# Optimization experiments

Hardware: AMD Instinct MI355X
Metric: run time of the kernel (lower is better)

Reference implementation:

```python
import jax, jax.numpy as jnp
import numpy as np

EPS = 0.1           # sinkhorn entropic regularizer (epsilon=0.1 in OT())
GAMMA = 1.0         # KL penalty on relaxed (row) marginal (gamma=1)
NUM_SK_ITERS = 3    # num_iters=3, final=False path
RHO_UPPER = 1.0
RHO_BASE = 0.1


def sigmoid_rampup(current, rampup_length):
    if rampup_length == 0:
        return 1.0
    current = np.clip(current, 0.0, rampup_length)
    phase = 1.0 - current / rampup_length
    return float(np.exp(-5.0 * phase * phase))


def set_rho(current, total):
    rho = sigmoid_rampup(current, total) * RHO_UPPER + RHO_BASE
    return min(rho, 1.0)


def setup_inputs() -> dict:
    key = jax.random.key(0)
    kx, ky = jax.random.split(key)
    x = jax.random.normal(kx, (8192, 1024), dtype=jnp.float32)
    y = jax.random.normal(ky, (2048, 1024), dtype=jnp.float32)
    return {"x": x, "y": y, "iterations": 100, "iterations_per_epoch": 20}


def _normalize_feature(x):
    # x = x - x.min(-1)[0].unsqueeze(-1)
    return x - jnp.min(x, axis=-1, keepdims=True)


def _cdist(x, y):
    # torch.cdist with p=2 (Euclidean)
    x2 = jnp.sum(x * x, axis=-1, keepdims=True)          # (N,1)
    y2 = jnp.sum(y * y, axis=-1)                         # (M,)
    d2 = x2 + y2[None, :] - 2.0 * (x @ y.T)              # (N,M)
    return jnp.sqrt(jnp.maximum(d2, 0.0))


def _semi_sinkhorn_stable(cost, rho):
    """Log-domain (stable) semi-relaxed Sinkhorn-Knopp.
    Column marginal is enforced exactly with total mass rho (curriculum mass);
    row marginal is relaxed via KL penalty gamma -> damped f update.
    Returns transport plan with sum(flow) == rho."""
    N, M = cost.shape
    lam = GAMMA / (GAMMA + EPS)
    loga = -np.log(N)                   # uniform row prior (prior=None)
    logb = np.log(rho) - np.log(M)      # uniform column marginal, mass rho
    logK = -cost / EPS                  # (N,M)
    f = jnp.zeros((N,), cost.dtype)
    g = jnp.zeros((M,), cost.dtype)
    lse = jax.scipy.special.logsumexp
    for _ in range(NUM_SK_ITERS):
        f = -lam * EPS * lse(logK + g[None, :] / EPS + logb, axis=1)
        g = -EPS * lse(logK + f[:, None] / EPS + loga, axis=0)
    flow = jnp.exp(logK + f[:, None] / EPS + g[None, :] / EPS + loga + logb)
    return flow


def reference(x, y, iterations, iterations_per_epoch):
    x = _normalize_feature(x)
    y = _normalize_feature(y)
    rho = set_rho(iterations, 10 * iterations_per_epoch)  # sigmoid rho schedule
    cost = _cdist(x, y)
    cost = cost / jnp.max(cost)
    flow = _semi_sinkhorn_stable(cost, rho)
    flow = flow / rho                                      # renormalize to total mass 1
    dist = jnp.sum(cost * flow)
    return flow, dist
```

## Files before the change

### kernel.cpp

```cpp
#include <hip/hip_runtime.h>
#include <math.h>

#define N_ROWS 8192
#define M_COLS 2048
#define K_DIM  1024
#define NM     ((size_t)N_ROWS * M_COLS)

#define LAM       0.9090909090909091f
#define LOG_M     7.624618986159398f

#define SKB 1024
#define RPB (N_ROWS / SKB)

typedef __bf16 bf16x8 __attribute__((ext_vector_type(8)));
typedef float  f32x4  __attribute__((ext_vector_type(4)));
typedef unsigned short u16x8 __attribute__((ext_vector_type(8)));
typedef _Float16 h8 __attribute__((ext_vector_type(8)));


static __device__ __forceinline__ size_t xb_off(int i) {
    return ((size_t)(i >> 1) << 13) + 4096 + ((size_t)(i & 1) << 11);
}
static __device__ __forceinline__ size_t yb_off(int j) {
    return ((size_t)1 << 25) + ((size_t)(j >> 1) << 13) + 4096 + ((size_t)(j & 1) << 11);
}

static __device__ __forceinline__ unsigned pk_bf16(float a, float b) {
#if __has_builtin(__builtin_amdgcn_cvt_pk_bf16_f32)
    typedef __bf16 bf16x2 __attribute__((ext_vector_type(2)));
    bf16x2 r = __builtin_amdgcn_cvt_pk_bf16_f32(a, b);
    return __builtin_bit_cast(unsigned, r);
#else
    unsigned ua = __float_as_uint(a), ub = __float_as_uint(b);
    ua += 0x7FFFu + ((ua >> 16) & 1u);
    ub += 0x7FFFu + ((ub >> 16) & 1u);
    return (ua >> 16) | (ub & 0xFFFF0000u);
#endif
}

static __device__ __forceinline__ bf16x8 lds_frag(const unsigned short* p) {
    return __builtin_bit_cast(bf16x8, *(const u16x8*)p);
}

static __device__ __forceinline__ void gload16(const void* g, void* l) {
    __builtin_amdgcn_global_load_lds(
        (const __attribute__((address_space(1))) unsigned int*)g,
        (__attribute__((address_space(3))) unsigned int*)l, 16, 0, 0);
}

__global__ __launch_bounds__(256) void rowstats_cvt(
    const float* __restrict__ X, const float* __restrict__ Y,
    unsigned char* __restrict__ outb,
    const int* __restrict__ iters, const int* __restrict__ ipe,
    float* __restrict__ params, float* __restrict__ sigma,
    unsigned int* __restrict__ d2max, float* __restrict__ dist,
    float* __restrict__ mx, float* __restrict__ sx, float* __restrict__ x2,
    float* __restrict__ my, float* __restrict__ sy, float* __restrict__ y2)
{
    const int b = blockIdx.x, tid = threadIdx.x;

    if (b == 0) {
        #pragma unroll 1
        for (int i = tid; i < 3 * M_COLS; i += 256) sigma[i] = 0.0f;
        if (tid == 0) {
            float ramp = 10.0f * (float)ipe[0];
            float rho;
            if (ramp == 0.0f) {
                rho = 1.1f;
            } else {
                float cur = fminf(fmaxf((float)iters[0], 0.0f), ramp);
                float phase = 1.0f - cur / ramp;
                rho = expf(-5.0f * phase * phase) + 0.1f;
            }
            rho = fminf(rho, 1.0f);
            params[0] = rho;
            params[1] = logf(rho) - LOG_M;
            *d2max = 0u;
            *dist = 0.0f;
        }
    }

    const bool isX = b < N_ROWS;
    const int row = isX ? b : b - N_ROWS;
    const float* src = isX ? (X + (size_t)row * K_DIM) : (Y + (size_t)row * K_DIM);
    const float4 v = ((const float4*)src)[tid];

    uint2 p; p.x = pk_bf16(v.x, v.y); p.y = pk_bf16(v.z, v.w);
    size_t off = isX ? xb_off(row) : yb_off(row);
    *(uint2*)(outb + off + (size_t)tid * 8) = p;

    float lmin = fminf(fminf(v.x, v.y), fminf(v.z, v.w));
    float lsum = v.x + v.y + v.z + v.w;
    float lsq  = v.x*v.x + v.y*v.y + v.z*v.z + v.w*v.w;

    __shared__ float rmin[256], rsum[256], rsq[256];
    rmin[tid] = lmin; rsum[tid] = lsum; rsq[tid] = lsq;
    __syncthreads();
    for (int s = 128; s > 0; s >>= 1) {
        if (tid < s) {
            rmin[tid] = fminf(rmin[tid], rmin[tid + s]);
            rsum[tid] += rsum[tid + s];
            rsq[tid]  += rsq[tid + s];
        }
        __syncthreads();
    }
    if (tid == 0) {
        float m = rmin[0], s = rsum[0], q = rsq[0];
        if (isX) { mx[row] = m; sx[row] = s; x2[row] = q - 2.f*m*s + (float)K_DIM*m*m; }
        else     { my[row] = m; sy[row] = s; y2[row] = q - 2.f*m*s + (float)K_DIM*m*m; }
    }
}

__global__ __launch_bounds__(256, 4) void gemm_cost_mfma(
    float* __restrict__ gbuf,
    const float* __restrict__ mx, const float* __restrict__ sx, const float* __restrict__ x2,
    const float* __restrict__ my, const float* __restrict__ sy, const float* __restrict__ y2,
    unsigned int* __restrict__ d2max)
{
    __shared__ unsigned short Ash[2][128 * 32];
    __shared__ unsigned short Bsh[2][128 * 32];
    __shared__ float rmax[256];

    const unsigned char* outb = (const unsigned char*)gbuf;
    const int tid   = threadIdx.x;
    const int lane  = tid & 63;
    const int wave  = tid >> 6;
    const int wi    = wave >> 1;
    const int wj    = wave & 1;
    const int row16 = lane & 15;
    const int quad  = lane >> 4;

    const int bid0 = blockIdx.y * 16 + blockIdx.x;
    const int bid  = (bid0 & 7) * 128 + (bid0 >> 3);
    const int i0 = (bid >> 4) * 128, j0 = (bid & 15) * 128;

    const int chA = (lane & 3) * 16;
    const unsigned char* pa[2];
    const unsigned char* pb[2];
    unsigned short* laA[2];
    unsigned short* lbB[2];
    #pragma unroll
    for (int p = 0; p < 2; ++p) {
        const int rt = (p * 4 + wave) * 16 + (lane >> 2);
        pa[p] = outb + xb_off(i0 + rt) + chA;
        pb[p] = outb + yb_off(j0 + rt) + chA;
        laA[p] = &Ash[0][(p * 4 + wave) * 512];
        lbB[p] = &Bsh[0][(p * 4 + wave) * 512];
    }

    f32x4 acc[4][4];
    #pragma unroll
    for (int u = 0; u < 4; ++u)
        #pragma unroll
        for (int v = 0; v < 4; ++v) acc[u][v] = (f32x4){0.f, 0.f, 0.f, 0.f};

#define STAGE(nb) do {                                        \
        gload16(pa[0], laA[0] + (nb) * 4096);                 \
        gload16(pa[1], laA[1] + (nb) * 4096);                 \
        gload16(pb[0], lbB[0] + (nb) * 4096);                 \
        gload16(pb[1], lbB[1] + (nb) * 4096);                 \
        pa[0] += 64; pa[1] += 64; pb[0] += 64; pb[1] += 64;   \
    } while (0)

#define COMPUTE(cb) do {                                                         \
        bf16x8 af[4], bfr[4];                                                    \
        _Pragma("unroll")                                                        \
        for (int t = 0; t < 4; ++t) {                                            \
            af[t]  = lds_frag(&Ash[cb][(wi * 64 + t * 16 + row16) * 32 + quad * 8]); \
            bfr[t] = lds_frag(&Bsh[cb][(wj * 64 + t * 16 + row16) * 32 + quad * 8]); \
        }                                                                        \
        _Pragma("unroll")                                                        \
        for (int ti = 0; ti < 4; ++ti)                                           \
            _Pragma("unroll")                                                    \
            for (int tj = 0; tj < 4; ++tj)                                       \
                acc[ti][tj] = __builtin_amdgcn_mfma_f32_16x16x32_bf16(           \
                    af[ti], bfr[tj], acc[ti][tj], 0, 0, 0);                      \
    } while (0)

    STAGE(0);
    __syncthreads();

#pragma unroll 1
    for (int it = 0; it < 15; ++it) {
        STAGE(1); COMPUTE(0); __syncthreads();
        STAGE(0); COMPUTE(1); __syncthreads();
    }
    STAGE(1); COMPUTE(0); __syncthreads();
    COMPUTE(1);

#undef STAGE
#undef COMPUTE

    _Float16* costh = (_Float16*)gbuf;
    float lmax = 0.0f;
    float myj[4], syj[4], yy[4];
    #pragma unroll
    for (int tj = 0; tj < 4; ++tj) {
        const int j = j0 + wj * 64 + tj * 16 + row16;
        myj[tj] = my[j]; syj[tj] = sy[j]; yy[tj] = y2[j];
    }
    #pragma unroll
    for (int ti = 0; ti < 4; ++ti) {
        #pragma unroll
        for (int reg = 0; reg < 4; ++reg) {
            const int i = i0 + wi * 64 + ti * 16 + quad * 4 + reg;
            const float mxi = mx[i], sxi = sx[i], xxi = x2[i];
            #pragma unroll
            for (int tj = 0; tj < 4; ++tj) {
                const int j = j0 + wj * 64 + tj * 16 + row16;
                float corr = mxi * syj[tj] + myj[tj] * sxi - (float)K_DIM * mxi * myj[tj];
                float d2 = xxi + yy[tj] - 2.0f * acc[ti][tj][reg] + 2.0f * corr;
                d2 = fmaxf(d2, 0.0f);
                lmax = fmaxf(lmax, d2);
                costh[(size_t)i * 4096 + j] = (_Float16)sqrtf(d2);
            }
        }
    }
    rmax[tid] = lmax;
    __syncthreads();
    for (int s = 128; s > 0; s >>= 1) {
        if (tid < s) rmax[tid] = fmaxf(rmax[tid], rmax[tid + s]);
        __syncthreads();
    }
    if (tid == 0) atomicMax(d2max, __float_as_uint(rmax[0]));
}

template<int IT>
__global__ __launch_bounds__(256, 4) void sk_pass(
    const float* __restrict__ outbuf, const float* __restrict__ sigma,
    _Float16* __restrict__ gpart, float* __restrict__ w,
    const float* __restrict__ params, const unsigned int* __restrict__ d2max)
{
    __shared__ _Float16 Esh[RPB * M_COLS];
    __shared__ float R[RPB][4];
    __shared__ float W[RPB];

    const int tid  = threadIdx.x;
    const int lane = tid & 63;
    const int wave = tid >> 6;
    const int r0   = blockIdx.x * RPB;
    const float logb = params[1];
    const float invC10 = 10.0f * rsqrtf(__uint_as_float(*d2max));

    float u8[8];
    if constexpr (IT == 0) {
        #pragma unroll
        for (int c = 0; c < 8; ++c) u8[c] = 1.0f;
    } else {
        const float* sg = sigma + (IT - 1) * M_COLS;
        const float4 sa = *(const float4*)(sg + 8 * tid);
        const float4 sb = *(const float4*)(sg + 8 * tid + 4);
        u8[0] = (float)N_ROWS / sa.x; u8[1] = (float)N_ROWS / sa.y;
        u8[2] = (float)N_ROWS / sa.z; u8[3] = (float)N_ROWS / sa.w;
        u8[4] = (float)N_ROWS / sb.x; u8[5] = (float)N_ROWS / sb.y;
        u8[6] = (float)N_ROWS / sb.z; u8[7] = (float)N_ROWS / sb.w;
    }

    const _Float16* Cb = (const _Float16*)outbuf;
    float pr[RPB];
    #pragma unroll
    for (int r = 0; r < RPB; ++r) {
        h8 c = __builtin_bit_cast(h8, *(const uint4*)(Cb + (size_t)(r0 + r) * 4096 + 8 * tid));
        h8 e;
        float s = 0.0f;
        #pragma unroll
        for (int k = 0; k < 8; ++k) {
            _Float16 ek = (_Float16)__expf(-(float)c[k] * invC10);
            e[k] = ek;
            s += (float)ek * u8[k];
        }
        *(uint4*)&Esh[r * M_COLS + 8 * tid] = __builtin_bit_cast(uint4, e);
        pr[r] = s;
    }

    #pragma unroll
    for (int r = 0; r < RPB; ++r)
        #pragma unroll
        for (int off = 32; off > 0; off >>= 1)
            pr[r] += __shfl_xor(pr[r], off, 64);

    if (lane == 0)
        #pragma unroll
        for (int r = 0; r < RPB; ++r) R[r][wave] = pr[r];
    __syncthreads();
    if (tid < RPB) {
        float t = R[tid][0] + R[tid][1] + R[tid][2] + R[tid][3];
        float wr = __expf(-LAM * (logb + __logf(t)));
        W[tid] = wr;
        if constexpr (IT == 2) w[r0 + tid] = wr;
    }
    __syncthreads();

    float p[8] = {0.f, 0.f, 0.f, 0.f, 0.f, 0.f, 0.f, 0.f};
    #pragma unroll
    for (int r = 0; r < RPB; ++r) {
        h8 e = __builtin_bit_cast(h8, *(const uint4*)&Esh[r * M_COLS + 8 * tid]);
        const float wr = W[r];
        #pragma unroll
        for (int k = 0; k < 8; ++k) p[k] += (float)e[k] * wr;
    }
    h8 ph;
    #pragma unroll
    for (int k = 0; k < 8; ++k) ph[k] = (_Float16)p[k];
    *(uint4*)(gpart + (size_t)blockIdx.x * M_COLS + 8 * tid) = __builtin_bit_cast(uint4, ph);
}

__global__ __launch_bounds__(256) void sk_gred(
    const _Float16* __restrict__ gpart, float* __restrict__ sigma)
{
    const int col = (blockIdx.x & 7) * 256 + threadIdx.x;
    const int b0  = (blockIdx.x >> 3) * (SKB / 16);
    float s = 0.0f;
    #pragma unroll 8
    for (int b = 0; b < SKB / 16; ++b)
        s += (float)gpart[(size_t)(b0 + b) * M_COLS + col];
    atomicAdd(&sigma[col], s);
}

__global__ __launch_bounds__(256, 4) void flow_dist(
    float* __restrict__ outbuf, const float* __restrict__ w,
    const float* __restrict__ sigma2, const unsigned int* __restrict__ d2max,
    float* __restrict__ dist)
{
    __shared__ _Float16 Csh[RPB * M_COLS];
    __shared__ float W[RPB];
    __shared__ float red[256];

    const int tid = threadIdx.x;
    const int r0  = blockIdx.x * RPB;
    const float invNM = 1.0f / ((float)N_ROWS * (float)M_COLS);
    const float invC10 = 10.0f * rsqrtf(__uint_as_float(*d2max));
    const float inv01  = 0.1f * invC10;
    const _Float16* Cb = (const _Float16*)outbuf;

    #pragma unroll
    for (int r = 0; r < RPB; ++r) {
        uint4 cv = *(const uint4*)(Cb + (size_t)(r0 + r) * 4096 + 8 * tid);
        *(uint4*)&Csh[r * M_COLS + 8 * tid] = cv;
    }

    if (tid < RPB) W[tid] = w[r0 + tid];

    const float4 sA = *(const float4*)(sigma2 + 8 * tid);
    const float4 sB = *(const float4*)(sigma2 + 8 * tid + 4);
    float u8[8];
    u8[0] = (float)N_ROWS / sA.x; u8[1] = (float)N_ROWS / sA.y;
    u8[2] = (float)N_ROWS / sA.z; u8[3] = (float)N_ROWS / sA.w;
    u8[4] = (float)N_ROWS / sB.x; u8[5] = (float)N_ROWS / sB.y;
    u8[6] = (float)N_ROWS / sB.z; u8[7] = (float)N_ROWS / sB.w;

    __syncthreads();

    float local = 0.0f;
    #pragma unroll
    for (int r = 0; r < RPB; ++r) {
        h8 c = __builtin_bit_cast(h8, *(const uint4*)&Csh[r * M_COLS + 8 * tid]);
        const float wr = W[r];
        float fl[8];
        #pragma unroll
        for (int k = 0; k < 8; ++k) {
            float cst = (float)c[k];
            float e = __expf(-cst * invC10);
            float o = e * wr * u8[k] * invNM;
            fl[k] = o;
            local += (cst * inv01) * o;
        }
        float4 o0 = {fl[0], fl[1], fl[2], fl[3]};
        float4 o1 = {fl[4], fl[5], fl[6], fl[7]};
        float* frow = outbuf + (size_t)(r0 + r) * M_COLS + 8 * tid;
        *(float4*)frow = o0;
        *(float4*)(frow + 4) = o1;
    }

    red[tid] = local;
    __syncthreads();
    for (int s = 128; s > 0; s >>= 1) {
        if (tid < s) red[tid] += red[tid + s];
        __syncthreads();
    }
    if (tid == 0) atomicAdd(dist, red[0]);
}

extern "C" void kernel_launch(void* const* d_in, const int* in_sizes, int n_in,
                              void* d_out, int out_size, void* d_ws, size_t ws_size,
                              hipStream_t stream)
{
    const float* x     = (const float*)d_in[0];
    const float* y     = (const float*)d_in[1];
    const int*   iters = (const int*)d_in[2];
    const int*   ipe   = (const int*)d_in[3];
    float* out = (float*)d_out;
    float* ws  = (float*)d_ws;

    float*        params = ws;
    unsigned int* d2max  = (unsigned int*)(ws + 8);
    float* w     = ws + 16;
    float* sigma = w + N_ROWS;
    float* mx = sigma + 3 * M_COLS;
    float* sx = mx + N_ROWS;
    float* x2 = sx + N_ROWS;
    float* my = x2 + N_ROWS;
    float* sy = my + M_COLS;
    float* y2 = sy + M_COLS;
    _Float16* gpart = (_Float16*)(y2 + M_COLS);

    float* sigma0 = sigma;
    float* sigma1 = sigma + M_COLS;
    float* sigma2 = sigma + 2 * M_COLS;

    float* dist = out + NM;

    rowstats_cvt<<<N_ROWS + M_COLS, 256, 0, stream>>>(
        x, y, (unsigned char*)out, iters, ipe, params, sigma, d2max, dist,
        mx, sx, x2, my, sy, y2);
    gemm_cost_mfma<<<dim3(M_COLS / 128, N_ROWS / 128), 256, 0, stream>>>(
        out, mx, sx, x2, my, sy, y2, d2max);

    sk_pass<0><<<SKB, 256, 0, stream>>>(out, sigma, gpart, w, params, d2max);
    sk_gred<<<128, 256, 0, stream>>>(gpart, sigma0);
    sk_pass<1><<<SKB, 256, 0, stream>>>(out, sigma, gpart, w, params, d2max);
    sk_gred<<<128, 256, 0, stream>>>(gpart, sigma1);
    sk_pass<2><<<SKB, 256, 0, stream>>>(out, sigma, gpart, w, params, d2max);
    sk_gred<<<128, 256, 0, stream>>>(gpart, sigma2);

    flow_dist<<<SKB, 256, 0, stream>>>(out, w, sigma2, d2max, dist);
}
```

Before: 215.8 us.

## Enlarge GEMM tiles to 256x256 with swizzled LDS and deeper K pipelining

The bf16 MFMA cost GEMM moves from 128x128 tiles with 256 threads and K-step 32 to 256x256 tiles with 512 threads and K-step 64. It adds an XOR-swizzled LDS layout to avoid bank conflicts, explicit vmcnt and lgkmcnt waits with raw barriers, and s_setprio around the MFMA bursts. The aim is more data reuse per global load and better overlap of loads with compute. The cost is much more LDS per block (128 KB) and more accumulator registers, which lowers occupancy. With 256 blocks, the grid roughly matches the CU count.

```diff
diff --git a/kernel.cpp b/kernel.cpp
--- a/kernel.cpp
+++ b/kernel.cpp
@@ -111,114 +111,132 @@
     }
 }
 
-__global__ __launch_bounds__(256, 4) void gemm_cost_mfma(
+__global__ __launch_bounds__(512, 2) void gemm_cost_mfma(
     float* __restrict__ gbuf,
     const float* __restrict__ mx, const float* __restrict__ sx, const float* __restrict__ x2,
     const float* __restrict__ my, const float* __restrict__ sy, const float* __restrict__ y2,
     unsigned int* __restrict__ d2max)
 {
-    __shared__ unsigned short Ash[2][128 * 32];
-    __shared__ unsigned short Bsh[2][128 * 32];
-    __shared__ float rmax[256];
+    __shared__ unsigned short Ash[2][256 * 64];
+    __shared__ unsigned short Bsh[2][256 * 64];
+    __shared__ float rmax[512];
 
     const unsigned char* outb = (const unsigned char*)gbuf;
-    const int tid   = threadIdx.x;
-    const int lane  = tid & 63;
-    const int wave  = tid >> 6;
-    const int wi    = wave >> 1;
-    const int wj    = wave & 1;
-    const int row16 = lane & 15;
-    const int quad  = lane >> 4;
-
-    const int bid0 = blockIdx.y * 16 + blockIdx.x;
-    const int bid  = (bid0 & 7) * 128 + (bid0 >> 3);
-    const int i0 = (bid >> 4) * 128, j0 = (bid & 15) * 128;
-
-    const int chA = (lane & 3) * 16;
-    const unsigned char* pa[2];
-    const unsigned char* pb[2];
-    unsigned short* laA[2];
-    unsigned short* lbB[2];
-    #pragma unroll
-    for (int p = 0; p < 2; ++p) {
-        const int rt = (p * 4 + wave) * 16 + (lane >> 2);
-        pa[p] = outb + xb_off(i0 + rt) + chA;
-        pb[p] = outb + yb_off(j0 + rt) + chA;
-        laA[p] = &Ash[0][(p * 4 + wave) * 512];
-        lbB[p] = &Bsh[0][(p * 4 + wave) * 512];
-    }
-
-    f32x4 acc[4][4];
-    #pragma unroll
-    for (int u = 0; u < 4; ++u)
+    const int tid  = threadIdx.x;
+    const int lane = tid & 63;
+    const int wave = tid >> 6;
+    const int wm   = wave >> 2;
+    const int wn   = wave & 3;
+    const int r16  = lane & 15;
+    const int q    = lane >> 4;
+
+    const int bid0 = blockIdx.x;
+    const int bid  = (bid0 & 7) * 32 + (bid0 >> 3);
+    const int i0 = (bid >> 3) * 256, j0 = (bid & 7) * 256;
+
+    const int srow  = tid >> 3;
+    const int sslot = tid & 7;
+    const int chS   = (sslot ^ (srow & 7)) * 16;
+
+    f32x4 acc[8][4];
+    #pragma unroll
+    for (int u = 0; u < 8; ++u)
         #pragma unroll
         for (int v = 0; v < 4; ++v) acc[u][v] = (f32x4){0.f, 0.f, 0.f, 0.f};
 
-#define STAGE(nb) do {                                        \
-        gload16(pa[0], laA[0] + (nb) * 4096);                 \
-        gload16(pa[1], laA[1] + (nb) * 4096);                 \
-        gload16(pb[0], lbB[0] + (nb) * 4096);                 \
-        gload16(pb[1], lbB[1] + (nb) * 4096);                 \
-        pa[0] += 64; pa[1] += 64; pb[0] += 64; pb[1] += 64;   \
+    bf16x8 af[8], bfr[4];
+
+#define STAGE(t2, s) do {                                                      \
+        const int kb = (t2) * 128;                                             \
+        _Pragma("unroll")                                                      \
+        for (int g = 0; g < 4; ++g) {                                          \
+            const int rw = g * 64 + srow;                                      \
+            gload16(outb + xb_off(i0 + rw) + kb + chS,                         \
+                    &Ash[s][g * 4096 + wave * 512]);                           \
+            gload16(outb + yb_off(j0 + rw) + kb + chS,                         \
+                    &Bsh[s][g * 4096 + wave * 512]);                           \
+        }                                                                      \
     } while (0)
 
-#define COMPUTE(cb) do {                                                         \
-        bf16x8 af[4], bfr[4];                                                    \
-        _Pragma("unroll")                                                        \
-        for (int t = 0; t < 4; ++t) {                                            \
-            af[t]  = lds_frag(&Ash[cb][(wi * 64 + t * 16 + row16) * 32 + quad * 8]); \
-            bfr[t] = lds_frag(&Bsh[cb][(wj * 64 + t * 16 + row16) * 32 + quad * 8]); \
-        }                                                                        \
-        _Pragma("unroll")                                                        \
-        for (int ti = 0; ti < 4; ++ti)                                           \
-            _Pragma("unroll")                                                    \
-            for (int tj = 0; tj < 4; ++tj)                                       \
-                acc[ti][tj] = __builtin_amdgcn_mfma_f32_16x16x32_bf16(           \
-                    af[ti], bfr[tj], acc[ti][tj], 0, 0, 0);                      \
+#define FRAGS(s, kk) do {                                                      \
+        _Pragma("unroll")                                                      \
+        for (int mi = 0; mi < 8; ++mi) {                                       \
+            const int rA = wm * 128 + mi * 16 + r16;                           \
+            af[mi] = lds_frag(&Ash[s][rA * 64 + (((kk)*4 + q) ^ (rA & 7)) * 8]); \
+        }                                                                      \
+        _Pragma("unroll")                                                      \
+        for (int ni = 0; ni < 4; ++ni) {                                       \
+            const int rB = wn * 64 + ni * 16 + r16;                            \
+            bfr[ni] = lds_frag(&Bsh[s][rB * 64 + (((kk)*4 + q) ^ (rB & 7)) * 8]); \
+        }                                                                      \
     } while (0)
 
-    STAGE(0);
-    __syncthreads();
-
-#pragma unroll 1
-    for (int it = 0; it < 15; ++it) {
-        STAGE(1); COMPUTE(0); __syncthreads();
-        STAGE(0); COMPUTE(1); __syncthreads();
-    }
-    STAGE(1); COMPUTE(0); __syncthreads();
-    COMPUTE(1);
+#define MMAS() do {                                                            \
+        _Pragma("unroll")                                                      \
+        for (int mi = 0; mi < 8; ++mi)                                         \
+            _Pragma("unroll")                                                  \
+            for (int ni = 0; ni < 4; ++ni)                                     \
+                acc[mi][ni] = __builtin_amdgcn_mfma_f32_16x16x32_bf16(         \
+                    af[mi], bfr[ni], acc[mi][ni], 0, 0, 0);                    \
+    } while (0)
+
+    STAGE(0, 0);
+    STAGE(1, 1);
+
+    #pragma unroll 1
+    for (int t = 0; t < 16; ++t) {
+        const int side = t & 1;
+        if (t < 15) asm volatile("s_waitcnt vmcnt(8)" ::: "memory");
+        else        asm volatile("s_waitcnt vmcnt(0)" ::: "memory");
+        __builtin_amdgcn_s_barrier();
+        __builtin_amdgcn_sched_barrier(0);
+
+        FRAGS(side, 0);
+        asm volatile("s_waitcnt lgkmcnt(0)" ::: "memory");
+        __builtin_amdgcn_sched_barrier(0);
+        __builtin_amdgcn_s_setprio(1); MMAS(); __builtin_amdgcn_s_setprio(0);
+
+        FRAGS(side, 1);
+        asm volatile("s_waitcnt lgkmcnt(0)" ::: "memory");
+        __builtin_amdgcn_sched_barrier(0);
+        __builtin_amdgcn_s_barrier();
+        __builtin_amdgcn_sched_barrier(0);
+        if (t <= 13) STAGE(t + 2, side);
+        __builtin_amdgcn_s_setprio(1); MMAS(); __builtin_amdgcn_s_setprio(0);
+    }
 
 #undef STAGE
-#undef COMPUTE
+#undef FRAGS
+#undef MMAS
 
     _Float16* costh = (_Float16*)gbuf;
     float lmax = 0.0f;
     float myj[4], syj[4], yy[4];
-    #pragma unroll
-    for (int tj = 0; tj < 4; ++tj) {
-        const int j = j0 + wj * 64 + tj * 16 + row16;
-        myj[tj] = my[j]; syj[tj] = sy[j]; yy[tj] = y2[j];
-    }
-    #pragma unroll
-    for (int ti = 0; ti < 4; ++ti) {
+    int jb[4];
+    #pragma unroll
+    for (int ni = 0; ni < 4; ++ni) {
+        jb[ni] = j0 + wn * 64 + ni * 16 + r16;
+        myj[ni] = my[jb[ni]]; syj[ni] = sy[jb[ni]]; yy[ni] = y2[jb[ni]];
+    }
+    #pragma unroll
+    for (int mi = 0; mi < 8; ++mi) {
         #pragma unroll
         for (int reg = 0; reg < 4; ++reg) {
-            const int i = i0 + wi * 64 + ti * 16 + quad * 4 + reg;
+            const int i = i0 + wm * 128 + mi * 16 + q * 4 + reg;
             const float mxi = mx[i], sxi = sx[i], xxi = x2[i];
             #pragma unroll
-            for (int tj = 0; tj < 4; ++tj) {
-                const int j = j0 + wj * 64 + tj * 16 + row16;
-                float corr = mxi * syj[tj] + myj[tj] * sxi - (float)K_DIM * mxi * myj[tj];
-                float d2 = xxi + yy[tj] - 2.0f * acc[ti][tj][reg] + 2.0f * corr;
+            for (int ni = 0; ni < 4; ++ni) {
+                float corr = mxi * syj[ni] + myj[ni] * sxi - (float)K_DIM * mxi * myj[ni];
+                float d2 = xxi + yy[ni] - 2.0f * acc[mi][ni][reg] + 2.0f * corr;
                 d2 = fmaxf(d2, 0.0f);
                 lmax = fmaxf(lmax, d2);
-                costh[(size_t)i * 4096 + j] = (_Float16)sqrtf(d2);
+                costh[(size_t)i * 4096 + jb[ni]] = (_Float16)sqrtf(d2);
             }
         }
     }
     rmax[tid] = lmax;
     __syncthreads();
-    for (int s = 128; s > 0; s >>= 1) {
+    for (int s = 256; s > 0; s >>= 1) {
         if (tid < s) rmax[tid] = fmaxf(rmax[tid], rmax[tid + s]);
         __syncthreads();
     }
@@ -413,7 +431,7 @@
     rowstats_cvt<<<N_ROWS + M_COLS, 256, 0, stream>>>(
         x, y, (unsigned char*)out, iters, ipe, params, sigma, d2max, dist,
         mx, sx, x2, my, sy, y2);
-    gemm_cost_mfma<<<dim3(M_COLS / 128, N_ROWS / 128), 256, 0, stream>>>(
+    gemm_cost_mfma<<<(N_ROWS / 256) * (M_COLS / 256), 512, 0, stream>>>(
         out, mx, sx, x2, my, sy, y2, d2max);
 
     sk_pass<0><<<SKB, 256, 0, stream>>>(out, sigma, gpart, w, params, d2max);
```

After: 207.6 us, median of 3. -3.8%, faster.
